# Kernel optimization log

Measured on AMD Instinct MI355X. Metric: run time of the kernel, lower is better.

Reference implementation:

```python
import jax, jax.numpy as jnp
import numpy as np

B, S, D, H = 2, 2048, 1024, 16


def setup_inputs() -> dict:
    key = jax.random.key(0)
    ks = jax.random.split(key, 8)
    wscale = 1.0 / np.sqrt(D)  # ~xavier for square matrices
    return {
        "q": jax.random.normal(ks[0], (B, S, D), jnp.float32),
        "k": jax.random.normal(ks[1], (B, S, D), jnp.float32),
        "v": jax.random.normal(ks[2], (B, S, D), jnp.float32),
        "mask": jnp.tril(jnp.ones((S, S), jnp.int32))[None, None, :, :],  # [1,1,S,S] causal
        "Wq": jax.random.normal(ks[3], (D, D), jnp.float32) * wscale,
        "bq": jnp.zeros((D,), jnp.float32),
        "Wk": jax.random.normal(ks[4], (D, D), jnp.float32) * wscale,
        "bk": jnp.zeros((D,), jnp.float32),
        "Wv": jax.random.normal(ks[5], (D, D), jnp.float32) * wscale,
        "bv": jnp.zeros((D,), jnp.float32),
        "Wo": jax.random.normal(ks[6], (D, D), jnp.float32) * wscale,
        "bo": jnp.zeros((D,), jnp.float32),
    }


def reference(q, k, v, mask, Wq, bq, Wk, bk, Wv, bv, Wo, bo):
    batch_size, seq_len = q.shape[0], q.shape[1]
    qp = q @ Wq + bq
    kp = k @ Wk + bk
    vp = v @ Wv + bv
    qkv = jnp.concatenate([qp, kp, vp], axis=2)          # [B,S,3D]
    qkv = jnp.reshape(qkv, (batch_size, seq_len, H, -1), order='F')  # faithful Fortran-order head split
    qkv = qkv.transpose(0, 2, 1, 3)                      # [B,H,S,3*hd]
    qh, kh, vh = jnp.array_split(qkv, 3, axis=-1)        # each [B,H,S,hd]
    scores = qh @ jnp.swapaxes(kh, -2, -1) / kh.shape[-1] ** 0.5  # [B,H,S,S]
    scores = jnp.where(mask == 0, -9e15, scores)
    attention = jax.nn.softmax(scores, axis=-1)
    values = attention @ vh                              # [B,H,S,hd]
    values = values.transpose(0, 2, 1, 3).reshape(batch_size, seq_len, D)
    out = values @ Wo + bo
    return (out, attention)
```

## Files before the change

kernel.cpp:

```cpp
#include <hip/hip_runtime.h>
#include <stdint.h>

#define B_ 2
#define S_ 2048
#define D_ 1024
#define H_ 16
#define HD_ 64
#define BS_ 4096

typedef __bf16 bf16_t;
typedef __attribute__((ext_vector_type(8))) __bf16 bf16x8;
typedef __attribute__((ext_vector_type(4))) float f32x4;

#define VMCNT0 asm volatile("s_waitcnt vmcnt(0)" ::: "memory")
#define LGKMCNT0 asm volatile("s_waitcnt lgkmcnt(0)" ::: "memory")

__device__ __forceinline__ void barrier_raw() {
  asm volatile("" ::: "memory");
  __builtin_amdgcn_s_barrier();
  asm volatile("" ::: "memory");
}

__device__ __forceinline__ bf16_t f2bf(float f) {
  union { float f; uint32_t u; } v; v.f = f;
  uint32_t r = v.u + 0x7FFFu + ((v.u >> 16) & 1u);
  union { uint16_t u; bf16_t b; } o; o.u = (uint16_t)(r >> 16);
  return o.b;
}

__device__ __forceinline__ void gload_lds16(const void* g, void* l) {
  __builtin_amdgcn_global_load_lds((const __attribute__((address_space(1))) void*)g,
                                   (__attribute__((address_space(3))) void*)l,
                                   16, 0, 0);
}

__device__ __forceinline__ void stage64(const bf16_t* __restrict__ g, int gstride,
                                        bf16_t* lds, int wave, int lane) {
  #pragma unroll
  for (int i = 0; i < 2; ++i) {
    int lin = (wave * 2 + i) * 64 + lane;
    int row = lin >> 3, c = lin & 7;
    gload_lds16(g + (size_t)row * gstride + ((c ^ (row & 7)) << 3), (char*)lds + lin * 16);
  }
}

__device__ __forceinline__ void stage128(const bf16_t* __restrict__ g, int gstride,
                                         bf16_t* lds, int wave, int lane) {
  #pragma unroll
  for (int i = 0; i < 4; ++i) {
    int lin = (wave * 4 + i) * 64 + lane;
    int row = lin >> 3, c = lin & 7;
    gload_lds16(g + (size_t)row * gstride + ((c ^ (row & 7)) << 3), (char*)lds + lin * 16);
  }
}

__device__ __forceinline__ bf16x8 frag64(const bf16_t* lds, int row, int chunk) {
  return *(const bf16x8*)((const char*)lds + row * 128 + ((chunk ^ (row & 7)) << 4));
}

__global__ __launch_bounds__(256) void to_bf16_3_kernel(const float* __restrict__ q,
                                                        const float* __restrict__ k,
                                                        const float* __restrict__ v,
                                                        bf16_t* __restrict__ qb,
                                                        bf16_t* __restrict__ kb,
                                                        bf16_t* __restrict__ vb) {
  const int which = blockIdx.y;
  const float* in = which == 0 ? q : which == 1 ? k : v;
  bf16_t* out = which == 0 ? qb : which == 1 ? kb : vb;
  int i = (blockIdx.x * 256 + threadIdx.x) * 8;
  const float4* p = (const float4*)(in + i);
  float4 a = p[0], b = p[1];
  bf16x8 o;
  o[0] = f2bf(a.x); o[1] = f2bf(a.y); o[2] = f2bf(a.z); o[3] = f2bf(a.w);
  o[4] = f2bf(b.x); o[5] = f2bf(b.y); o[6] = f2bf(b.z); o[7] = f2bf(b.w);
  *(bf16x8*)(out + i) = o;
}

__global__ __launch_bounds__(256) void conv_weight4_kernel(const float* __restrict__ Wq,
                                                           const float* __restrict__ Wk,
                                                           const float* __restrict__ Wv,
                                                           const float* __restrict__ Wo,
                                                           bf16_t* __restrict__ wt_base) {
  const int which = blockIdx.z;
  const float* w = which == 0 ? Wq : which == 1 ? Wk : which == 2 ? Wv : Wo;
  bf16_t* wt = wt_base + (size_t)which * D_ * D_;
  const int permute = (which < 3) ? 1 : 0;
  const float scale = (which == 0) ? 0.125f : 1.0f;

  __shared__ float tile[64][65];
  int d0 = blockIdx.x * 64, o0 = blockIdx.y * 64;
  #pragma unroll
  for (int it = 0; it < 16; ++it) {
    int e = it * 256 + threadIdx.x;
    int r = e >> 6, c = e & 63;
    tile[r][c] = w[(size_t)(d0 + r) * D_ + o0 + c];
  }
  __syncthreads();
  #pragma unroll
  for (int it = 0; it < 16; ++it) {
    int e = it * 256 + threadIdx.x;
    int dd = e & 63, oo = e >> 6;
    int o = o0 + oo;
    int np = permute ? ((o & 15) * 64 + (o >> 4)) : o;
    wt[(size_t)np * D_ + d0 + dd] = f2bf(tile[dd][oo] * scale);
  }
}

__global__ __launch_bounds__(256) void perm_bias_kernel(const float* __restrict__ bq,
                                                        const float* __restrict__ bk,
                                                        const float* __restrict__ bv,
                                                        float* __restrict__ out) {
  int i = blockIdx.x * 256 + threadIdx.x;
  if (i >= 3 * D_) return;
  int which = i >> 10, n = i & 1023;
  int src = (n >> 6) + ((n & 63) << 4);
  const float* b = which == 0 ? bq : (which == 1 ? bk : bv);
  out[i] = b[src] * (which == 0 ? 0.125f : 1.0f);
}

__global__ __launch_bounds__(256) void gemm_qkv_kernel(const bf16_t* __restrict__ Aq,
                                                       const bf16_t* __restrict__ Ak,
                                                       const bf16_t* __restrict__ Av,
                                                       const bf16_t* __restrict__ Bt,
                                                       const float* __restrict__ bias,
                                                       bf16_t* __restrict__ Oq,
                                                       bf16_t* __restrict__ Ok,
                                                       bf16_t* __restrict__ Ov) {
  __shared__ bf16_t As[128 * 64];
  __shared__ bf16_t Bs[128 * 64];
  const int tid = threadIdx.x, wave = tid >> 6, lane = tid & 63;
  const int wm = wave >> 1, wn = wave & 1;
  const int lrow = lane & 15, kgrp = lane >> 4;
  const int row0 = blockIdx.x * 128;
  const int which = blockIdx.y >> 3;
  const int col0 = (blockIdx.y & 7) * 128;
  const bf16_t* A = which == 0 ? Aq : which == 1 ? Ak : Av;
  bf16_t* O = which == 0 ? Oq : which == 1 ? Ok : Ov;
  const bf16_t* Brow = Bt + (size_t)(which * 1024 + col0) * 1024;
  const float* bs = bias + which * 1024 + col0;

  f32x4 acc[4][4];
  #pragma unroll
  for (int i = 0; i < 4; ++i)
    #pragma unroll
    for (int j = 0; j < 4; ++j) acc[i][j] = (f32x4){0.f, 0.f, 0.f, 0.f};

  for (int k0 = 0; k0 < 1024; k0 += 64) {
    __syncthreads();
    stage128(A + (size_t)row0 * 1024 + k0, 1024, As, wave, lane);
    stage128(Brow + k0, 1024, Bs, wave, lane);
    VMCNT0;
    __syncthreads();
    #pragma unroll
    for (int kk = 0; kk < 2; ++kk) {
      bf16x8 af[4], bfv[4];
      #pragma unroll
      for (int mi = 0; mi < 4; ++mi) af[mi] = frag64(As, wm * 64 + mi * 16 + lrow, kk * 4 + kgrp);
      #pragma unroll
      for (int nj = 0; nj < 4; ++nj) bfv[nj] = frag64(Bs, wn * 64 + nj * 16 + lrow, kk * 4 + kgrp);
      #pragma unroll
      for (int mi = 0; mi < 4; ++mi)
        #pragma unroll
        for (int nj = 0; nj < 4; ++nj)
          acc[mi][nj] = __builtin_amdgcn_mfma_f32_16x16x32_bf16(af[mi], bfv[nj], acc[mi][nj], 0, 0, 0);
    }
  }

  #pragma unroll
  for (int mi = 0; mi < 4; ++mi)
    #pragma unroll
    for (int nj = 0; nj < 4; ++nj) {
      const int col = wn * 64 + nj * 16 + lrow;
      const float bv = bs[col];
      #pragma unroll
      for (int r = 0; r < 4; ++r) {
        const int row = row0 + wm * 64 + mi * 16 + kgrp * 4 + r;
        O[(size_t)row * 1024 + col0 + col] = f2bf(acc[mi][nj][r] + bv);
      }
    }
}

__global__ __launch_bounds__(256) void gemm_out_kernel(const bf16_t* __restrict__ A,
                                                       const bf16_t* __restrict__ Bt,
                                                       const float* __restrict__ bias,
                                                       float* __restrict__ Cout) {
  __shared__ bf16_t As[128 * 64];
  __shared__ bf16_t Bs[64 * 64];
  const int tid = threadIdx.x, wave = tid >> 6, lane = tid & 63;
  const int wm = wave >> 1, wn = wave & 1;
  const int lrow = lane & 15, kgrp = lane >> 4;
  const int row0 = blockIdx.x * 128;
  const int col0 = blockIdx.y * 64;

  f32x4 acc[4][2];
  #pragma unroll
  for (int i = 0; i < 4; ++i)
    #pragma unroll
    for (int j = 0; j < 2; ++j) acc[i][j] = (f32x4){0.f, 0.f, 0.f, 0.f};

  for (int k0 = 0; k0 < 1024; k0 += 64) {
    __syncthreads();
    stage128(A + (size_t)row0 * 1024 + k0, 1024, As, wave, lane);
    stage64(Bt + (size_t)col0 * 1024 + k0, 1024, Bs, wave, lane);
    VMCNT0;
    __syncthreads();
    #pragma unroll
    for (int kk = 0; kk < 2; ++kk) {
      bf16x8 af[4], bfv[2];
      #pragma unroll
      for (int mi = 0; mi < 4; ++mi) af[mi] = frag64(As, wm * 64 + mi * 16 + lrow, kk * 4 + kgrp);
      #pragma unroll
      for (int nj = 0; nj < 2; ++nj) bfv[nj] = frag64(Bs, wn * 32 + nj * 16 + lrow, kk * 4 + kgrp);
      #pragma unroll
      for (int mi = 0; mi < 4; ++mi)
        #pragma unroll
        for (int nj = 0; nj < 2; ++nj)
          acc[mi][nj] = __builtin_amdgcn_mfma_f32_16x16x32_bf16(af[mi], bfv[nj], acc[mi][nj], 0, 0, 0);
    }
  }

  #pragma unroll
  for (int mi = 0; mi < 4; ++mi)
    #pragma unroll
    for (int nj = 0; nj < 2; ++nj) {
      const int col = col0 + wn * 32 + nj * 16 + lrow;
      const float bv = bias[col];
      #pragma unroll
      for (int r = 0; r < 4; ++r) {
        const int row = row0 + wm * 64 + mi * 16 + kgrp * 4 + r;
        Cout[(size_t)row * 1024 + col] = acc[mi][nj][r] + bv;
      }
    }
}

__global__ __launch_bounds__(256) void transpose_v_kernel(const bf16_t* __restrict__ Vp,
                                                          bf16_t* __restrict__ Vt) {
  __shared__ bf16_t t[64][80];
  const int st = blockIdx.x, bh = blockIdx.y;
  const int b = bh >> 4, h = bh & 15;
  const int tid = threadIdx.x;
  #pragma unroll
  for (int i = 0; i < 2; ++i) {
    int lin = i * 256 + tid;
    int r = lin >> 3, c = (lin & 7) * 8;
    bf16x8 v8 = *(const bf16x8*)(Vp + ((size_t)(b * S_ + st * 64 + r)) * D_ + h * HD_ + c);
    *(bf16x8*)&t[r][c] = v8;
  }
  __syncthreads();
  #pragma unroll
  for (int i = 0; i < 2; ++i) {
    int lin = i * 256 + tid;
    int f = lin >> 3, c = (lin & 7) * 8;
    bf16x8 o;
    #pragma unroll
    for (int e = 0; e < 8; ++e) o[e] = t[c + e][f];
    *(bf16x8*)(Vt + ((size_t)bh * HD_ + f) * S_ + st * 64 + c) = o;
  }
}

__global__ __launch_bounds__(256, 4) void attn_kernel(const bf16_t* __restrict__ Q,
                                                      const bf16_t* __restrict__ K,
                                                      const bf16_t* __restrict__ Vt,
                                                      float* __restrict__ attn_out,
                                                      bf16_t* __restrict__ values) {
  __shared__ bf16_t KsB[2][64 * 64];
  __shared__ bf16_t VtsB[2][64 * 64];
  __shared__ bf16_t Ps[4][16 * 64];

  const int tid = threadIdx.x;
  const int wave = tid >> 6, lane = tid & 63;
  const int lrow = lane & 15, kgrp = lane >> 4;
  const int bh = blockIdx.y, b = bh >> 4, h = bh & 15;
  const size_t base = (size_t)b * S_ * D_ + (size_t)h * HD_;
  const size_t vbase = (size_t)bh * HD_ * S_;
  const int qt = (31 - (int)blockIdx.x + bh) & 31;
  const int qr0 = qt * 64;
  bf16_t* psw = &Ps[wave][0];

  const bf16_t* qp = Q + base + (size_t)(qr0 + wave * 16 + lrow) * D_ + kgrp * 8;
  bf16x8 aq[2];
  aq[0] = *(const bf16x8*)qp;
  aq[1] = *(const bf16x8*)(qp + 32);

  stage64(K + base, D_, KsB[0], wave, lane);
  VMCNT0; barrier_raw();

  float psum[4] = {0.f, 0.f, 0.f, 0.f};
  for (int kj = 0; kj <= qt; ++kj) {
    if (kj < qt) stage64(K + base + (size_t)(kj + 1) * 64 * D_, D_, KsB[(kj + 1) & 1], wave, lane);
    const bf16_t* Kc = KsB[kj & 1];
    f32x4 s[4];
    #pragma unroll
    for (int nj = 0; nj < 4; ++nj) {
      s[nj] = (f32x4){0.f, 0.f, 0.f, 0.f};
      #pragma unroll
      for (int kk = 0; kk < 2; ++kk)
        s[nj] = __builtin_amdgcn_mfma_f32_16x16x32_bf16(
            aq[kk], frag64(Kc, nj * 16 + lrow, kk * 4 + kgrp), s[nj], 0, 0, 0);
    }
    if (kj == qt) {
      #pragma unroll
      for (int nj = 0; nj < 4; ++nj)
        #pragma unroll
        for (int r = 0; r < 4; ++r) {
          int lrq = wave * 16 + kgrp * 4 + r;
          int lck = nj * 16 + lrow;
          psum[r] += (lck > lrq) ? 0.f : __expf(s[nj][r]);
        }
    } else {
      #pragma unroll
      for (int nj = 0; nj < 4; ++nj)
        #pragma unroll
        for (int r = 0; r < 4; ++r) psum[r] += __expf(s[nj][r]);
    }
    VMCNT0; barrier_raw();
  }

  float rl[4];
  #pragma unroll
  for (int r = 0; r < 4; ++r) {
    float t = psum[r];
    #pragma unroll
    for (int off = 1; off < 16; off <<= 1) t += __shfl_xor(t, off);
    rl[r] = 1.0f / t;
  }

  f32x4 o[4];
  #pragma unroll
  for (int nj = 0; nj < 4; ++nj) o[nj] = (f32x4){0.f, 0.f, 0.f, 0.f};

  stage64(K + base, D_, KsB[0], wave, lane);
  stage64(Vt + vbase, S_, VtsB[0], wave, lane);
  VMCNT0; barrier_raw();

  for (int kj = 0; kj <= qt; ++kj) {
    if (kj < qt) {
      stage64(K + base + (size_t)(kj + 1) * 64 * D_, D_, KsB[(kj + 1) & 1], wave, lane);
      stage64(Vt + vbase + (kj + 1) * 64, S_, VtsB[(kj + 1) & 1], wave, lane);
    }
    __builtin_amdgcn_sched_barrier(0);
    const bf16_t* Kc = KsB[kj & 1];
    const bf16_t* Vc = VtsB[kj & 1];
    f32x4 s[4];
    #pragma unroll
    for (int nj = 0; nj < 4; ++nj) {
      s[nj] = (f32x4){0.f, 0.f, 0.f, 0.f};
      #pragma unroll
      for (int kk = 0; kk < 2; ++kk)
        s[nj] = __builtin_amdgcn_mfma_f32_16x16x32_bf16(
            aq[kk], frag64(Kc, nj * 16 + lrow, kk * 4 + kgrp), s[nj], 0, 0, 0);
    }
    float* gpb = attn_out + ((size_t)bh * S_ + qr0 + wave * 16 + kgrp * 4) * S_ + kj * 64;
    #pragma unroll
    for (int nj = 0; nj < 4; ++nj)
      #pragma unroll
      for (int r = 0; r < 4; ++r) {
        int lrq = wave * 16 + kgrp * 4 + r;
        int lck = nj * 16 + lrow;
        float p = __expf(s[nj][r]) * rl[r];
        if (kj == qt && lck > lrq) p = 0.f;
        gpb[(size_t)r * S_ + nj * 16 + lrow] = p;
        {
          int prow = kgrp * 4 + r, pcol = nj * 16 + lrow;
          *(bf16_t*)((char*)psw + prow * 128 + (((pcol >> 3) ^ (prow & 7)) << 4) + (pcol & 7) * 2) = f2bf(p);
        }
      }
    LGKMCNT0;

    bf16x8 pa[2];
    #pragma unroll
    for (int kk = 0; kk < 2; ++kk)
      pa[kk] = *(const bf16x8*)((const char*)psw + lrow * 128 + (((kk * 4 + kgrp) ^ (lrow & 7)) << 4));
    #pragma unroll
    for (int nj = 0; nj < 4; ++nj)
      #pragma unroll
      for (int kk = 0; kk < 2; ++kk)
        o[nj] = __builtin_amdgcn_mfma_f32_16x16x32_bf16(
            pa[kk], frag64(Vc, nj * 16 + lrow, kk * 4 + kgrp), o[nj], 0, 0, 0);

    asm volatile("s_waitcnt vmcnt(16)" ::: "memory");
    barrier_raw();
  }

  {
    const int cstart = (qt + 1) * 64;
    if (cstart < S_) {
      int r = tid >> 2;
      float4 z = make_float4(0.f, 0.f, 0.f, 0.f);
      float* rowp = attn_out + ((size_t)bh * S_ + qr0 + r) * S_;
      for (int c = cstart + (tid & 3) * 4; c < S_; c += 16) *(float4*)(rowp + c) = z;
    }
  }

  #pragma unroll
  for (int nj = 0; nj < 4; ++nj)
    #pragma unroll
    for (int r = 0; r < 4; ++r) {
      int grow = qr0 + wave * 16 + kgrp * 4 + r;
      values[(size_t)(b * S_ + grow) * D_ + h * HD_ + nj * 16 + lrow] = f2bf(o[nj][r]);
    }
}

extern "C" void kernel_launch(void* const* d_in, const int* in_sizes, int n_in,
                              void* d_out, int out_size, void* d_ws, size_t ws_size,
                              hipStream_t stream) {
  const float* q  = (const float*)d_in[0];
  const float* k  = (const float*)d_in[1];
  const float* v  = (const float*)d_in[2];
  const float* Wq = (const float*)d_in[4];
  const float* bq = (const float*)d_in[5];
  const float* Wk = (const float*)d_in[6];
  const float* bk = (const float*)d_in[7];
  const float* Wv = (const float*)d_in[8];
  const float* bv = (const float*)d_in[9];
  const float* Wo = (const float*)d_in[10];
  const float* bo = (const float*)d_in[11];

  char* ws = (char*)d_ws;
  bf16_t* qb    = (bf16_t*)ws;
  bf16_t* kb    = qb + (size_t)BS_ * D_;
  bf16_t* vb    = kb + (size_t)BS_ * D_;
  bf16_t* Wqt   = vb + (size_t)BS_ * D_;
  bf16_t* Wkt   = Wqt + (size_t)D_ * D_;
  bf16_t* Wvt   = Wkt + (size_t)D_ * D_;
  bf16_t* Wot   = Wvt + (size_t)D_ * D_;
  float*  bias3 = (float*)(Wot + (size_t)D_ * D_);
  bf16_t* Qp    = (bf16_t*)(bias3 + 3 * D_);
  bf16_t* Kp    = Qp + (size_t)BS_ * D_;
  bf16_t* Vp    = Kp + (size_t)BS_ * D_;
  bf16_t* Vt    = qb;
  bf16_t* Val   = kb;

  to_bf16_3_kernel<<<dim3(2048, 3), 256, 0, stream>>>(q, k, v, qb, kb, vb);
  conv_weight4_kernel<<<dim3(16, 16, 4), 256, 0, stream>>>(Wq, Wk, Wv, Wo, Wqt);
  perm_bias_kernel<<<12, 256, 0, stream>>>(bq, bk, bv, bias3);

  gemm_qkv_kernel<<<dim3(32, 24), 256, 0, stream>>>(qb, kb, vb, Wqt, bias3, Qp, Kp, Vp);
  transpose_v_kernel<<<dim3(32, 32), 256, 0, stream>>>(Vp, Vt);

  float* attn_out = (float*)d_out + (size_t)BS_ * D_;
  attn_kernel<<<dim3(32, 32), 256, 0, stream>>>(Qp, Kp, Vt, attn_out, Val);

  gemm_out_kernel<<<dim3(32, 16), 256, 0, stream>>>(Val, Wot, bo, (float*)d_out);
}
```

Measured before the change: 302.5 us.

## Use 32x32x16 MFMA with transposed S and register-resident P in attention

Rewrites the attention kernel to use 2 waves per block, each covering 32 query rows. It computes S^T with 32x32x16 bf16 MFMA so each lane owns one query row. The probabilities are packed to bf16 with v_cvt_pk_bf16_f32 and rearranged with v_permlane32_swap, so they feed the PV MFMA straight from registers. This removes the LDS round-trip for P and the cross-lane row-sum shuffles, and lets the attention matrix be written as float4 vectors. The cost is fewer waves per block, a larger per-thread register footprint, and possibly lower occupancy.

```diff
diff --git a/kernel.cpp b/kernel.cpp
--- a/kernel.cpp
+++ b/kernel.cpp
@@ -11,6 +11,7 @@
 typedef __bf16 bf16_t;
 typedef __attribute__((ext_vector_type(8))) __bf16 bf16x8;
 typedef __attribute__((ext_vector_type(4))) float f32x4;
+typedef __attribute__((ext_vector_type(16))) float f32x16;
 
 #define VMCNT0 asm volatile("s_waitcnt vmcnt(0)" ::: "memory")
 #define LGKMCNT0 asm volatile("s_waitcnt lgkmcnt(0)" ::: "memory")
@@ -28,6 +29,14 @@
   return o.b;
 }
 
+__device__ __forceinline__ uint32_t cvtpk_bf16(float lo, float hi) {
+  uint32_t r;
+  asm("v_cvt_pk_bf16_f32 %0, %1, %2" : "=v"(r) : "v"(lo), "v"(hi));
+  return r;
+}
+
+#define PLSWAP(a, b) asm volatile("v_permlane32_swap_b32 %0, %1" : "+v"(a), "+v"(b))
+
 __device__ __forceinline__ void gload_lds16(const void* g, void* l) {
   __builtin_amdgcn_global_load_lds((const __attribute__((address_space(1))) void*)g,
                                    (__attribute__((address_space(3))) void*)l,
@@ -39,6 +48,16 @@
   #pragma unroll
   for (int i = 0; i < 2; ++i) {
     int lin = (wave * 2 + i) * 64 + lane;
+    int row = lin >> 3, c = lin & 7;
+    gload_lds16(g + (size_t)row * gstride + ((c ^ (row & 7)) << 3), (char*)lds + lin * 16);
+  }
+}
+
+__device__ __forceinline__ void stage64_2w(const bf16_t* __restrict__ g, int gstride,
+                                           bf16_t* lds, int tid) {
+  #pragma unroll
+  for (int i = 0; i < 4; ++i) {
+    int lin = i * 128 + tid;
     int row = lin >> 3, c = lin & 7;
     gload_lds16(g + (size_t)row * gstride + ((c ^ (row & 7)) << 3), (char*)lds + lin * 16);
   }
@@ -258,147 +277,141 @@
   }
 }
 
-__global__ __launch_bounds__(256, 4) void attn_kernel(const bf16_t* __restrict__ Q,
+__global__ __launch_bounds__(128, 2) void attn_kernel(const bf16_t* __restrict__ Q,
                                                       const bf16_t* __restrict__ K,
                                                       const bf16_t* __restrict__ Vt,
                                                       float* __restrict__ attn_out,
                                                       bf16_t* __restrict__ values) {
   __shared__ bf16_t KsB[2][64 * 64];
   __shared__ bf16_t VtsB[2][64 * 64];
-  __shared__ bf16_t Ps[4][16 * 64];
 
   const int tid = threadIdx.x;
   const int wave = tid >> 6, lane = tid & 63;
-  const int lrow = lane & 15, kgrp = lane >> 4;
+  const int lq = lane & 31, hi = lane >> 5;
   const int bh = blockIdx.y, b = bh >> 4, h = bh & 15;
   const size_t base = (size_t)b * S_ * D_ + (size_t)h * HD_;
   const size_t vbase = (size_t)bh * HD_ * S_;
   const int qt = (31 - (int)blockIdx.x + bh) & 31;
   const int qr0 = qt * 64;
-  bf16_t* psw = &Ps[wave][0];
-
-  const bf16_t* qp = Q + base + (size_t)(qr0 + wave * 16 + lrow) * D_ + kgrp * 8;
-  bf16x8 aq[2];
-  aq[0] = *(const bf16x8*)qp;
-  aq[1] = *(const bf16x8*)(qp + 32);
-
-  stage64(K + base, D_, KsB[0], wave, lane);
+  const int qrow = qr0 + wave * 32 + lq;
+
+  bf16x8 qf[4];
+  #pragma unroll
+  for (int dd = 0; dd < 4; ++dd)
+    qf[dd] = *(const bf16x8*)(Q + base + (size_t)qrow * D_ + dd * 16 + hi * 8);
+
+  stage64_2w(K + base, D_, KsB[0], tid);
   VMCNT0; barrier_raw();
 
-  float psum[4] = {0.f, 0.f, 0.f, 0.f};
+  float psum = 0.f;
   for (int kj = 0; kj <= qt; ++kj) {
-    if (kj < qt) stage64(K + base + (size_t)(kj + 1) * 64 * D_, D_, KsB[(kj + 1) & 1], wave, lane);
+    if (kj < qt) stage64_2w(K + base + (size_t)(kj + 1) * 64 * D_, D_, KsB[(kj + 1) & 1], tid);
     const bf16_t* Kc = KsB[kj & 1];
-    f32x4 s[4];
-    #pragma unroll
-    for (int nj = 0; nj < 4; ++nj) {
-      s[nj] = (f32x4){0.f, 0.f, 0.f, 0.f};
-      #pragma unroll
-      for (int kk = 0; kk < 2; ++kk)
-        s[nj] = __builtin_amdgcn_mfma_f32_16x16x32_bf16(
-            aq[kk], frag64(Kc, nj * 16 + lrow, kk * 4 + kgrp), s[nj], 0, 0, 0);
-    }
-    if (kj == qt) {
-      #pragma unroll
-      for (int nj = 0; nj < 4; ++nj)
-        #pragma unroll
-        for (int r = 0; r < 4; ++r) {
-          int lrq = wave * 16 + kgrp * 4 + r;
-          int lck = nj * 16 + lrow;
-          psum[r] += (lck > lrq) ? 0.f : __expf(s[nj][r]);
+    #pragma unroll
+    for (int kh = 0; kh < 2; ++kh) {
+      f32x16 S;
+      #pragma unroll
+      for (int z = 0; z < 16; ++z) S[z] = 0.f;
+      #pragma unroll
+      for (int dd = 0; dd < 4; ++dd)
+        S = __builtin_amdgcn_mfma_f32_32x32x16_bf16(
+            frag64(Kc, kh * 32 + lq, dd * 2 + hi), qf[dd], S, 0, 0, 0);
+      if (kj == qt) {
+        #pragma unroll
+        for (int rg = 0; rg < 16; ++rg) {
+          int kg = kj * 64 + kh * 32 + (rg & 3) + 8 * (rg >> 2) + 4 * hi;
+          psum += (kg > qrow) ? 0.f : __expf(S[rg]);
         }
-    } else {
-      #pragma unroll
-      for (int nj = 0; nj < 4; ++nj)
-        #pragma unroll
-        for (int r = 0; r < 4; ++r) psum[r] += __expf(s[nj][r]);
+      } else {
+        #pragma unroll
+        for (int rg = 0; rg < 16; ++rg) psum += __expf(S[rg]);
+      }
     }
     VMCNT0; barrier_raw();
   }
-
-  float rl[4];
-  #pragma unroll
-  for (int r = 0; r < 4; ++r) {
-    float t = psum[r];
-    #pragma unroll
-    for (int off = 1; off < 16; off <<= 1) t += __shfl_xor(t, off);
-    rl[r] = 1.0f / t;
-  }
-
-  f32x4 o[4];
-  #pragma unroll
-  for (int nj = 0; nj < 4; ++nj) o[nj] = (f32x4){0.f, 0.f, 0.f, 0.f};
-
-  stage64(K + base, D_, KsB[0], wave, lane);
-  stage64(Vt + vbase, S_, VtsB[0], wave, lane);
+  psum += __shfl_xor(psum, 32);
+  const float rl = 1.0f / psum;
+
+  f32x16 oacc0, oacc1;
+  #pragma unroll
+  for (int z = 0; z < 16; ++z) { oacc0[z] = 0.f; oacc1[z] = 0.f; }
+
+  stage64_2w(K + base, D_, KsB[0], tid);
+  stage64_2w(Vt + vbase, S_, VtsB[0], tid);
   VMCNT0; barrier_raw();
 
   for (int kj = 0; kj <= qt; ++kj) {
     if (kj < qt) {
-      stage64(K + base + (size_t)(kj + 1) * 64 * D_, D_, KsB[(kj + 1) & 1], wave, lane);
-      stage64(Vt + vbase + (kj + 1) * 64, S_, VtsB[(kj + 1) & 1], wave, lane);
+      stage64_2w(K + base + (size_t)(kj + 1) * 64 * D_, D_, KsB[(kj + 1) & 1], tid);
+      stage64_2w(Vt + vbase + (kj + 1) * 64, S_, VtsB[(kj + 1) & 1], tid);
     }
     __builtin_amdgcn_sched_barrier(0);
     const bf16_t* Kc = KsB[kj & 1];
     const bf16_t* Vc = VtsB[kj & 1];
-    f32x4 s[4];
-    #pragma unroll
-    for (int nj = 0; nj < 4; ++nj) {
-      s[nj] = (f32x4){0.f, 0.f, 0.f, 0.f};
-      #pragma unroll
-      for (int kk = 0; kk < 2; ++kk)
-        s[nj] = __builtin_amdgcn_mfma_f32_16x16x32_bf16(
-            aq[kk], frag64(Kc, nj * 16 + lrow, kk * 4 + kgrp), s[nj], 0, 0, 0);
-    }
-    float* gpb = attn_out + ((size_t)bh * S_ + qr0 + wave * 16 + kgrp * 4) * S_ + kj * 64;
-    #pragma unroll
-    for (int nj = 0; nj < 4; ++nj)
-      #pragma unroll
-      for (int r = 0; r < 4; ++r) {
-        int lrq = wave * 16 + kgrp * 4 + r;
-        int lck = nj * 16 + lrow;
-        float p = __expf(s[nj][r]) * rl[r];
-        if (kj == qt && lck > lrq) p = 0.f;
-        gpb[(size_t)r * S_ + nj * 16 + lrow] = p;
-        {
-          int prow = kgrp * 4 + r, pcol = nj * 16 + lrow;
-          *(bf16_t*)((char*)psw + prow * 128 + (((pcol >> 3) ^ (prow & 7)) << 4) + (pcol & 7) * 2) = f2bf(p);
+    #pragma unroll
+    for (int kh = 0; kh < 2; ++kh) {
+      f32x16 S;
+      #pragma unroll
+      for (int z = 0; z < 16; ++z) S[z] = 0.f;
+      #pragma unroll
+      for (int dd = 0; dd < 4; ++dd)
+        S = __builtin_amdgcn_mfma_f32_32x32x16_bf16(
+            frag64(Kc, kh * 32 + lq, dd * 2 + hi), qf[dd], S, 0, 0, 0);
+
+      float p[16];
+      if (kj == qt) {
+        #pragma unroll
+        for (int rg = 0; rg < 16; ++rg) {
+          int kg = kj * 64 + kh * 32 + (rg & 3) + 8 * (rg >> 2) + 4 * hi;
+          float pv = __expf(S[rg]) * rl;
+          p[rg] = (kg > qrow) ? 0.f : pv;
         }
+      } else {
+        #pragma unroll
+        for (int rg = 0; rg < 16; ++rg) p[rg] = __expf(S[rg]) * rl;
       }
-    LGKMCNT0;
-
-    bf16x8 pa[2];
-    #pragma unroll
-    for (int kk = 0; kk < 2; ++kk)
-      pa[kk] = *(const bf16x8*)((const char*)psw + lrow * 128 + (((kk * 4 + kgrp) ^ (lrow & 7)) << 4));
-    #pragma unroll
-    for (int nj = 0; nj < 4; ++nj)
-      #pragma unroll
-      for (int kk = 0; kk < 2; ++kk)
-        o[nj] = __builtin_amdgcn_mfma_f32_16x16x32_bf16(
-            pa[kk], frag64(Vc, nj * 16 + lrow, kk * 4 + kgrp), o[nj], 0, 0, 0);
-
-    asm volatile("s_waitcnt vmcnt(16)" ::: "memory");
+
+      float* gp = attn_out + ((size_t)bh * S_ + qrow) * S_ + kj * 64 + kh * 32 + 4 * hi;
+      #pragma unroll
+      for (int g = 0; g < 4; ++g)
+        *(float4*)(gp + 8 * g) = make_float4(p[4 * g], p[4 * g + 1], p[4 * g + 2], p[4 * g + 3]);
+
+      #pragma unroll
+      for (int ks = 0; ks < 2; ++ks) {
+        uint32_t w0 = cvtpk_bf16(p[8 * ks + 0], p[8 * ks + 1]);
+        uint32_t w1 = cvtpk_bf16(p[8 * ks + 2], p[8 * ks + 3]);
+        uint32_t w2 = cvtpk_bf16(p[8 * ks + 4], p[8 * ks + 5]);
+        uint32_t w3 = cvtpk_bf16(p[8 * ks + 6], p[8 * ks + 7]);
+        PLSWAP(w0, w2);
+        PLSWAP(w1, w3);
+        union { uint32_t u[4]; bf16x8 v; } pf;
+        pf.u[0] = w0; pf.u[1] = w1; pf.u[2] = w2; pf.u[3] = w3;
+        const int vch = kh * 4 + ks * 2 + hi;
+        oacc0 = __builtin_amdgcn_mfma_f32_32x32x16_bf16(pf.v, frag64(Vc, lq, vch), oacc0, 0, 0, 0);
+        oacc1 = __builtin_amdgcn_mfma_f32_32x32x16_bf16(pf.v, frag64(Vc, 32 + lq, vch), oacc1, 0, 0, 0);
+      }
+    }
+    asm volatile("s_waitcnt vmcnt(8)" ::: "memory");
     barrier_raw();
   }
 
   {
     const int cstart = (qt + 1) * 64;
     if (cstart < S_) {
-      int r = tid >> 2;
+      int r = tid >> 1;
       float4 z = make_float4(0.f, 0.f, 0.f, 0.f);
       float* rowp = attn_out + ((size_t)bh * S_ + qr0 + r) * S_;
-      for (int c = cstart + (tid & 3) * 4; c < S_; c += 16) *(float4*)(rowp + c) = z;
-    }
-  }
-
-  #pragma unroll
-  for (int nj = 0; nj < 4; ++nj)
-    #pragma unroll
-    for (int r = 0; r < 4; ++r) {
-      int grow = qr0 + wave * 16 + kgrp * 4 + r;
-      values[(size_t)(b * S_ + grow) * D_ + h * HD_ + nj * 16 + lrow] = f2bf(o[nj][r]);
-    }
+      for (int c = cstart + (tid & 1) * 4; c < S_; c += 8) *(float4*)(rowp + c) = z;
+    }
+  }
+
+  #pragma unroll
+  for (int rg = 0; rg < 16; ++rg) {
+    int qloc = (rg & 3) + 8 * (rg >> 2) + 4 * hi;
+    size_t rowoff = (size_t)(b * S_ + qr0 + wave * 32 + qloc) * D_ + h * HD_;
+    values[rowoff + lq] = f2bf(oacc0[rg]);
+    values[rowoff + 32 + lq] = f2bf(oacc1[rg]);
+  }
 }
 
 extern "C" void kernel_launch(void* const* d_in, const int* in_sizes, int n_in,
@@ -439,7 +452,7 @@
   transpose_v_kernel<<<dim3(32, 32), 256, 0, stream>>>(Vp, Vt);
 
   float* attn_out = (float*)d_out + (size_t)BS_ * D_;
-  attn_kernel<<<dim3(32, 32), 256, 0, stream>>>(Qp, Kp, Vt, attn_out, Val);
+  attn_kernel<<<dim3(32, 32), 128, 0, stream>>>(Qp, Kp, Vt, attn_out, Val);
 
   gemm_out_kernel<<<dim3(32, 16), 256, 0, stream>>>(Val, Wot, bo, (float*)d_out);
 }
```

After: 327.7 us. 1.08x slower.
